# Kernel tuning notes

Hardware: AMD Instinct MI355X
Metric: run time of the kernel (lower is better)

Reference implementation:

```python
import jax, jax.numpy as jnp
import numpy as np

NUM_HEADS = 16
LN_EPS = 1e-05


def setup_inputs() -> dict:
    key = jax.random.key(0)
    ks = jax.random.split(key, 10)
    B, S, H = 2, 2048, 1024
    s = 1.0 / np.sqrt(H)
    return {
        "hidden_states": jax.random.normal(ks[0], (B, S, H), dtype=jnp.float32),
        "Wq": jax.random.normal(ks[1], (H, H), dtype=jnp.float32) * s,
        "bq": jax.random.normal(ks[2], (H,), dtype=jnp.float32) * 0.02,
        "Wk": jax.random.normal(ks[3], (H, H), dtype=jnp.float32) * s,
        "bk": jax.random.normal(ks[4], (H,), dtype=jnp.float32) * 0.02,
        "Wv": jax.random.normal(ks[5], (H, H), dtype=jnp.float32) * s,
        "bv": jax.random.normal(ks[6], (H,), dtype=jnp.float32) * 0.02,
        "Wd": jax.random.normal(ks[7], (H, H), dtype=jnp.float32) * s,
        "bd": jax.random.normal(ks[8], (H,), dtype=jnp.float32) * 0.02,
        "ln_gamma": jnp.ones((H,), dtype=jnp.float32),
        "ln_beta": jnp.zeros((H,), dtype=jnp.float32),
    }


def reference(hidden_states, Wq, bq, Wk, bk, Wv, bv, Wd, bd, ln_gamma, ln_beta):
    B, S, H = hidden_states.shape
    nh = NUM_HEADS
    hd = H // nh

    # QKV projections (torch Linear: x @ W.T + b), split heads -> [B, nh, S, hd]
    def proj(W, b):
        y = jnp.einsum('bsh,oh->bso', hidden_states, W) + b
        return y.reshape(B, S, nh, hd).transpose(0, 2, 1, 3)

    q = proj(Wq, bq)
    k = proj(Wk, bk)
    v = proj(Wv, bv)

    # scaled dot-product attention: [B, nh, S, S]
    scores = jnp.einsum('bhqd,bhkd->bhqk', q, k) / jnp.sqrt(jnp.float32(hd))
    probs = jax.nn.softmax(scores, axis=-1)
    ctx = jnp.einsum('bhqk,bhkd->bhqd', probs, v)  # [B, nh, S, hd]
    ctx = ctx.transpose(0, 2, 1, 3).reshape(B, S, H)

    # output dense + residual + LayerNorm
    attn_out = jnp.einsum('bsh,oh->bso', ctx, Wd) + bd
    x = attn_out + hidden_states
    mu = jnp.mean(x, axis=-1, keepdims=True)
    var = jnp.mean(jnp.square(x - mu), axis=-1, keepdims=True)
    return (x - mu) * jax.lax.rsqrt(var + LN_EPS) * ln_gamma + ln_beta
```

## Files before the change

kernel.cpp:

```cpp
#include <hip/hip_runtime.h>

constexpr int kH    = 1024;
constexpr int kSEQ  = 2048;
constexpr int kBATCH= 2;
constexpr int kNH   = 16;
constexpr int kHD   = 64;
constexpr int kM    = 4096;

typedef _Float16 h8  __attribute__((ext_vector_type(8)));
typedef _Float16 h4  __attribute__((ext_vector_type(4)));
typedef float   f32x4 __attribute__((ext_vector_type(4)));

static __device__ __forceinline__ f32x4 mfma16(h8 a, h8 b, f32x4 c) {
  return __builtin_amdgcn_mfma_f32_16x16x32_f16(a, b, c, 0, 0, 0);
}

static __device__ __forceinline__ void gll16(const _Float16* g, _Float16* l) {
  __builtin_amdgcn_global_load_lds(
      (const __attribute__((address_space(1))) void*)g,
      (__attribute__((address_space(3))) void*)l, 16, 0, 0);
}

#define QSCALE 0.18033688011112042f
#define C0INIT (-5.770780163555854f)

__global__ __launch_bounds__(256) void cvt_all(
    const float* __restrict__ X,  const float* __restrict__ Wq,
    const float* __restrict__ Wk, const float* __restrict__ Wv,
    const float* __restrict__ Wd,
    _Float16* __restrict__ Xh,  _Float16* __restrict__ Wqh,
    _Float16* __restrict__ Wkh, _Float16* __restrict__ Wvh,
    _Float16* __restrict__ Wdh)
{
  int i = blockIdx.x * 256 + threadIdx.x;
  const float* src; _Float16* dst; int off;
  if (i < (kM * kH) / 4) {
    src = X; dst = Xh; off = i;
  } else {
    int j = i - (kM * kH) / 4;
    int w = j >> 18;
    off = j & 262143;
    src = (w == 0) ? Wq : (w == 1) ? Wk : (w == 2) ? Wv : Wd;
    dst = (w == 0) ? Wqh : (w == 1) ? Wkh : (w == 2) ? Wvh : Wdh;
  }
  float4 v = reinterpret_cast<const float4*>(src)[off];
  h4 o;
  o[0] = (_Float16)v.x; o[1] = (_Float16)v.y;
  o[2] = (_Float16)v.z; o[3] = (_Float16)v.w;
  reinterpret_cast<h4*>(dst)[off] = o;
}

__global__ __launch_bounds__(256, 2) void qkv_gemm(
    const _Float16* __restrict__ Xh,
    const _Float16* __restrict__ Wq, const _Float16* __restrict__ Wk,
    const _Float16* __restrict__ Wv,
    const float* __restrict__ bq, const float* __restrict__ bk,
    const float* __restrict__ bv,
    _Float16* __restrict__ Qo, _Float16* __restrict__ Ko, _Float16* __restrict__ Vo)
{
  const int proj = blockIdx.z;
  const _Float16* W   = (proj == 0) ? Wq : ((proj == 1) ? Wk : Wv);
  const float*    bias= (proj == 0) ? bq : ((proj == 1) ? bk : bv);
  _Float16*       Out = (proj == 0) ? Qo : ((proj == 1) ? Ko : Vo);

  const int m0 = blockIdx.y * 128, n0 = blockIdx.x * 128;
  __shared__ __align__(16) _Float16 As[2][128 * 32];
  __shared__ __align__(16) _Float16 Bs[2][128 * 32];

  const int tid  = threadIdx.x;
  const int wave = tid >> 6, lane = tid & 63, quad = lane >> 4, l16 = lane & 15;
  const int mw = (wave & 1) * 64, nw = (wave >> 1) * 64;

  f32x4 acc[4][4] = {};
  const int grow = wave * 32 + (lane >> 2);
  const int gcol = (lane & 3) * 8;
  const _Float16* Ag = Xh + (size_t)(m0 + grow) * kH + gcol;
  const _Float16* Bg = W  + (size_t)(n0 + grow) * kH + gcol;

  {
    gll16(Ag,            &As[0][wave * 1024]);
    gll16(Ag + 16 * kH,  &As[0][wave * 1024 + 512]);
    gll16(Bg,            &Bs[0][wave * 1024]);
    gll16(Bg + 16 * kH,  &Bs[0][wave * 1024 + 512]);
  }

  for (int k = 0; k < 32; ++k) {
    const int cur = k & 1;
    __syncthreads();
    if (k < 31) {
      const int k0 = (k + 1) * 32, nb = cur ^ 1;
      gll16(Ag + k0,           &As[nb][wave * 1024]);
      gll16(Ag + 16 * kH + k0, &As[nb][wave * 1024 + 512]);
      gll16(Bg + k0,           &Bs[nb][wave * 1024]);
      gll16(Bg + 16 * kH + k0, &Bs[nb][wave * 1024 + 512]);
    }
    h8 af[4], bf[4];
    #pragma unroll
    for (int mi = 0; mi < 4; ++mi)
      af[mi] = *reinterpret_cast<const h8*>(&As[cur][(mw + mi * 16 + l16) * 32 + quad * 8]);
    #pragma unroll
    for (int ni = 0; ni < 4; ++ni)
      bf[ni] = *reinterpret_cast<const h8*>(&Bs[cur][(nw + ni * 16 + l16) * 32 + quad * 8]);
    #pragma unroll
    for (int mi = 0; mi < 4; ++mi)
      #pragma unroll
      for (int ni = 0; ni < 4; ++ni)
        acc[mi][ni] = mfma16(af[mi], bf[ni], acc[mi][ni]);
  }

  #pragma unroll
  for (int mi = 0; mi < 4; ++mi)
  #pragma unroll
  for (int ni = 0; ni < 4; ++ni) {
    const int ng = n0 + nw + ni * 16 + l16;
    const float bv_ = bias[ng];
    const int hh = ng >> 6, dd = ng & 63;
    #pragma unroll
    for (int r = 0; r < 4; ++r) {
      const int mg = m0 + mw + mi * 16 + quad * 4 + r;
      float val = acc[mi][ni][r] + bv_;
      if (proj == 0) val *= QSCALE;
      const int bb = mg >> 11, srow = mg & 2047;
      Out[(((size_t)(bb * kNH + hh) * kSEQ) + srow) * kHD + dd] = (_Float16)val;
    }
  }
}

__global__ __launch_bounds__(256) void vtrans(const _Float16* __restrict__ V,
                                              _Float16* __restrict__ Vt)
{
  const int st = blockIdx.x;
  const int bh = blockIdx.y;
  __shared__ __align__(16) _Float16 Lt[64][72];
  const int t = threadIdx.x, r = t >> 2, c = (t & 3) * 16;
  const _Float16* src = V + (size_t)bh * kSEQ * kHD + (size_t)(st * 64 + r) * kHD + c;
  h8 p0 = *reinterpret_cast<const h8*>(src);
  h8 p1 = *reinterpret_cast<const h8*>(src + 8);
  #pragma unroll
  for (int e = 0; e < 8; ++e) Lt[c + e][r] = p0[e];
  #pragma unroll
  for (int e = 0; e < 8; ++e) Lt[c + 8 + e][r] = p1[e];
  __syncthreads();
  _Float16* dst = Vt + (size_t)bh * kHD * kSEQ + (size_t)r * kSEQ + st * 64 + c;
  *reinterpret_cast<h8*>(dst)     = *reinterpret_cast<const h8*>(&Lt[r][c]);
  *reinterpret_cast<h8*>(dst + 8) = *reinterpret_cast<const h8*>(&Lt[r][c + 8]);
}

__global__ __launch_bounds__(512, 4) void attn_kernel(
    const _Float16* __restrict__ Q, const _Float16* __restrict__ K,
    const _Float16* __restrict__ Vt, _Float16* __restrict__ Ctx)
{
  const int qt = blockIdx.x, bh = blockIdx.y;
  const int tid = threadIdx.x;
  const int wave = tid >> 6, lane = tid & 63, quad = lane >> 4, l16 = lane & 15;
  const int sw = l16 & 7;

  __shared__ __align__(16) _Float16 Kl[2][64 * 64];
  __shared__ __align__(16) _Float16 Vl[2][64 * 64];
  __shared__ __align__(16) _Float16 Pl[8][16 * 64];

  const _Float16* Qb = Q  + (size_t)bh * kSEQ * kHD;
  const _Float16* Kb = K  + (size_t)bh * kSEQ * kHD;
  const _Float16* Vb = Vt + (size_t)bh * kHD * kSEQ;

  const int qbase = qt * 128 + wave * 16;
  h8 qf[2];
  #pragma unroll
  for (int dh = 0; dh < 2; ++dh)
    qf[dh] = *reinterpret_cast<const h8*>(
        &Qb[(size_t)(qbase + l16) * kHD + dh * 32 + quad * 8]);

  const int srow0  = lane >> 3;
  const int schunk = (lane & 7) ^ srow0;
  const int krow   = wave * 8 + srow0;
  const _Float16* Kg = Kb + (size_t)krow * kHD + schunk * 8;
  const _Float16* Vg = Vb + (size_t)krow * kSEQ + schunk * 8;
  _Float16* PlW = Pl[wave];

  float l_acc = 0.f;
  f32x4 o[4] = {};

  {
    gll16(Kg, &Kl[0][(wave * 8) * 64]);
    gll16(Vg, &Vl[0][(wave * 8) * 64]);
  }

  for (int kt = 0; kt < kSEQ / 64; ++kt) {
    const int cur = kt & 1;
    __syncthreads();
    if (kt + 1 < kSEQ / 64) {
      const int nb = cur ^ 1;
      const size_t ko = (size_t)(kt + 1) * 64;
      gll16(Kg + ko * kHD, &Kl[nb][(wave * 8) * 64]);
      gll16(Vg + ko,       &Vl[nb][(wave * 8) * 64]);
    }
    const _Float16* Kc = Kl[cur];
    const _Float16* Vc = Vl[cur];

    h8 ka[4][2];
    #pragma unroll
    for (int nt = 0; nt < 4; ++nt) {
      const int keyl = nt * 16 + l16;
      ka[nt][0] = *reinterpret_cast<const h8*>(&Kc[keyl * 64 + ((quad     ) ^ sw) * 8]);
      ka[nt][1] = *reinterpret_cast<const h8*>(&Kc[keyl * 64 + ((quad ^ 4) ^ sw) * 8]);
    }
    f32x4 s[4];
    __builtin_amdgcn_s_setprio(1);
    #pragma unroll
    for (int nt = 0; nt < 4; ++nt) {
      f32x4 a = {C0INIT, C0INIT, C0INIT, C0INIT};
      a = mfma16(ka[nt][0], qf[0], a);
      a = mfma16(ka[nt][1], qf[1], a);
      s[nt] = a;
    }
    __builtin_amdgcn_s_setprio(0);

    #pragma unroll
    for (int nt = 0; nt < 4; ++nt) {
      float e0 = exp2f(s[nt][0]);
      float e1 = exp2f(s[nt][1]);
      float e2 = exp2f(s[nt][2]);
      float e3 = exp2f(s[nt][3]);
      l_acc += (e0 + e1) + (e2 + e3);
      h4 pp;
      pp[0] = (_Float16)e0; pp[1] = (_Float16)e1;
      pp[2] = (_Float16)e2; pp[3] = (_Float16)e3;
      const int c8 = (nt * 2 + (quad >> 1)) ^ sw;
      *reinterpret_cast<h4*>(&PlW[l16 * 64 + c8 * 8 + (quad & 1) * 4]) = pp;
    }

    #pragma unroll
    for (int kc = 0; kc < 2; ++kc) {
      const int cs = ((kc * 4 + quad) ^ sw) * 8;
      h8 pa = *reinterpret_cast<const h8*>(&PlW[l16 * 64 + cs]);
      h8 vb0 = *reinterpret_cast<const h8*>(&Vc[(0 * 16 + l16) * 64 + cs]);
      h8 vb1 = *reinterpret_cast<const h8*>(&Vc[(1 * 16 + l16) * 64 + cs]);
      h8 vb2 = *reinterpret_cast<const h8*>(&Vc[(2 * 16 + l16) * 64 + cs]);
      h8 vb3 = *reinterpret_cast<const h8*>(&Vc[(3 * 16 + l16) * 64 + cs]);
      __builtin_amdgcn_s_setprio(1);
      o[0] = mfma16(pa, vb0, o[0]);
      o[1] = mfma16(pa, vb1, o[1]);
      o[2] = mfma16(pa, vb2, o[2]);
      o[3] = mfma16(pa, vb3, o[3]);
      __builtin_amdgcn_s_setprio(0);
    }
  }

  float li = l_acc;
  li += __shfl_xor(li, 16);
  li += __shfl_xor(li, 32);
  li = 1.f / li;
  const int b = bh >> 4, hh = bh & 15;
  #pragma unroll
  for (int r = 0; r < 4; ++r) {
    const float linv = __shfl(li, quad * 4 + r);
    const int srow = qbase + quad * 4 + r;
    #pragma unroll
    for (int dt = 0; dt < 4; ++dt) {
      const int col = hh * kHD + dt * 16 + l16;
      Ctx[((size_t)(b * kSEQ + srow)) * kH + col] = (_Float16)(o[dt][r] * linv);
    }
  }
}

__global__ __launch_bounds__(256, 2) void dense_gemm(
    const _Float16* __restrict__ A, const _Float16* __restrict__ W,
    const float* __restrict__ bias, const float* __restrict__ resid,
    float* __restrict__ Out)
{
  const int m0 = blockIdx.y * 128, n0 = blockIdx.x * 64;
  __shared__ __align__(16) _Float16 As[2][128 * 32];
  __shared__ __align__(16) _Float16 Bs[2][64 * 32];
  const int tid  = threadIdx.x;
  const int wave = tid >> 6, lane = tid & 63, quad = lane >> 4, l16 = lane & 15;
  const int mw = (wave & 1) * 64, nw = (wave >> 1) * 32;
  f32x4 acc[4][2] = {};
  const int growA = wave * 32 + (lane >> 2);
  const int growB = wave * 16 + (lane >> 2);
  const int gcol = (lane & 3) * 8;
  const _Float16* Ag = A + (size_t)(m0 + growA) * kH + gcol;
  const _Float16* Bg = W + (size_t)(n0 + growB) * kH + gcol;

  {
    gll16(Ag,           &As[0][wave * 1024]);
    gll16(Ag + 16 * kH, &As[0][wave * 1024 + 512]);
    gll16(Bg,           &Bs[0][wave * 512]);
  }

  for (int k = 0; k < 32; ++k) {
    const int cur = k & 1;
    __syncthreads();
    if (k < 31) {
      const int k0 = (k + 1) * 32, nb = cur ^ 1;
      gll16(Ag + k0,           &As[nb][wave * 1024]);
      gll16(Ag + 16 * kH + k0, &As[nb][wave * 1024 + 512]);
      gll16(Bg + k0,           &Bs[nb][wave * 512]);
    }
    h8 af[4], bf[2];
    #pragma unroll
    for (int mi = 0; mi < 4; ++mi)
      af[mi] = *reinterpret_cast<const h8*>(&As[cur][(mw + mi * 16 + l16) * 32 + quad * 8]);
    #pragma unroll
    for (int ni = 0; ni < 2; ++ni)
      bf[ni] = *reinterpret_cast<const h8*>(&Bs[cur][(nw + ni * 16 + l16) * 32 + quad * 8]);
    #pragma unroll
    for (int mi = 0; mi < 4; ++mi)
      #pragma unroll
      for (int ni = 0; ni < 2; ++ni)
        acc[mi][ni] = mfma16(af[mi], bf[ni], acc[mi][ni]);
  }
  #pragma unroll
  for (int mi = 0; mi < 4; ++mi)
  #pragma unroll
  for (int ni = 0; ni < 2; ++ni) {
    const int ng = n0 + nw + ni * 16 + l16;
    const float bv_ = bias[ng];
    #pragma unroll
    for (int r = 0; r < 4; ++r) {
      const int mg = m0 + mw + mi * 16 + quad * 4 + r;
      Out[(size_t)mg * kH + ng] = acc[mi][ni][r] + bv_ + resid[(size_t)mg * kH + ng];
    }
  }
}

__global__ __launch_bounds__(256) void ln_kernel(const float* __restrict__ Tmp,
    const float* __restrict__ gamma, const float* __restrict__ beta,
    float* __restrict__ out)
{
  const int row = blockIdx.x;
  const float4 v = reinterpret_cast<const float4*>(Tmp + (size_t)row * kH)[threadIdx.x];
  float s  = v.x + v.y + v.z + v.w;
  float ss = v.x * v.x + v.y * v.y + v.z * v.z + v.w * v.w;
  #pragma unroll
  for (int off = 32; off > 0; off >>= 1) {
    s  += __shfl_down(s, off);
    ss += __shfl_down(ss, off);
  }
  __shared__ float red[8];
  const int wave = threadIdx.x >> 6, lane = threadIdx.x & 63;
  if (lane == 0) { red[wave] = s; red[4 + wave] = ss; }
  __syncthreads();
  s  = red[0] + red[1] + red[2] + red[3];
  ss = red[4] + red[5] + red[6] + red[7];
  const float mu   = s * (1.f / kH);
  const float var  = ss * (1.f / kH) - mu * mu;
  const float rstd = rsqrtf(var + 1e-5f);
  const float4 g  = reinterpret_cast<const float4*>(gamma)[threadIdx.x];
  const float4 bb = reinterpret_cast<const float4*>(beta)[threadIdx.x];
  float4 o;
  o.x = (v.x - mu) * rstd * g.x + bb.x;
  o.y = (v.y - mu) * rstd * g.y + bb.y;
  o.z = (v.z - mu) * rstd * g.z + bb.z;
  o.w = (v.w - mu) * rstd * g.w + bb.w;
  reinterpret_cast<float4*>(out + (size_t)row * kH)[threadIdx.x] = o;
}

extern "C" void kernel_launch(void* const* d_in, const int* in_sizes, int n_in,
                              void* d_out, int out_size, void* d_ws, size_t ws_size,
                              hipStream_t stream) {
  const float* hs    = (const float*)d_in[0];
  const float* Wq    = (const float*)d_in[1];
  const float* bq    = (const float*)d_in[2];
  const float* Wk    = (const float*)d_in[3];
  const float* bk    = (const float*)d_in[4];
  const float* Wv    = (const float*)d_in[5];
  const float* bv    = (const float*)d_in[6];
  const float* Wd    = (const float*)d_in[7];
  const float* bd    = (const float*)d_in[8];
  const float* gamma = (const float*)d_in[9];
  const float* beta  = (const float*)d_in[10];
  float* out = (float*)d_out;

  char* ws = (char*)d_ws;
  _Float16* Xh  = (_Float16*)(ws + 0);
  _Float16* Wqh = (_Float16*)(ws + 8388608);
  _Float16* Wkh = (_Float16*)(ws + 10485760);
  _Float16* Wvh = (_Float16*)(ws + 12582912);
  _Float16* Wdh = (_Float16*)(ws + 14680064);
  _Float16* Qh  = (_Float16*)(ws + 16777216);
  _Float16* Kh  = (_Float16*)(ws + 25165824);
  _Float16* Vh  = (_Float16*)(ws + 33554432);
  _Float16* Ch  = (_Float16*)(ws + 41943040);
  _Float16* Vtb = Xh;
  float*    Tmp = (float*)Qh;

  cvt_all<<<8192, 256, 0, stream>>>(hs, Wq, Wk, Wv, Wd, Xh, Wqh, Wkh, Wvh, Wdh);
  qkv_gemm<<<dim3(kH / 128, kM / 128, 3), 256, 0, stream>>>(
      Xh, Wqh, Wkh, Wvh, bq, bk, bv, Qh, Kh, Vh);
  vtrans<<<dim3(kSEQ / 64, kBATCH * kNH), 256, 0, stream>>>(Vh, Vtb);
  attn_kernel<<<dim3(kSEQ / 128, kBATCH * kNH), 512, 0, stream>>>(Qh, Kh, Vtb, Ch);
  dense_gemm<<<dim3(kH / 64, kM / 128), 256, 0, stream>>>(Ch, Wdh, bd, hs, Tmp);
  ln_kernel<<<kM, 256, 0, stream>>>(Tmp, gamma, beta, out);
}
```

Before: 220.2 us.

## Split attention key tile across wave groups with 32-row queries and LDS reduction

```diff
diff --git a/kernel.cpp b/kernel.cpp
--- a/kernel.cpp
+++ b/kernel.cpp
@@ -154,36 +154,41 @@
   const int tid = threadIdx.x;
   const int wave = tid >> 6, lane = tid & 63, quad = lane >> 4, l16 = lane & 15;
   const int sw = l16 & 7;
-
-  __shared__ __align__(16) _Float16 Kl[2][64 * 64];
-  __shared__ __align__(16) _Float16 Vl[2][64 * 64];
-  __shared__ __align__(16) _Float16 Pl[8][16 * 64];
+  const int qw = wave & 3;
+  const int wg = wave >> 2;
+
+  __shared__ __align__(16) char smem[53248];
+  _Float16* const Kl = (_Float16*)smem;
+  _Float16* const Vl = (_Float16*)(smem + 16384);
+  _Float16* const Pl = (_Float16*)(smem + 32768);
+  float* const Ored = (float*)smem;
+  float* const Lred = (float*)(smem + 34816);
 
   const _Float16* Qb = Q  + (size_t)bh * kSEQ * kHD;
   const _Float16* Kb = K  + (size_t)bh * kSEQ * kHD;
   const _Float16* Vb = Vt + (size_t)bh * kHD * kSEQ;
 
-  const int qbase = qt * 128 + wave * 16;
-  h8 qf[2];
-  #pragma unroll
-  for (int dh = 0; dh < 2; ++dh)
-    qf[dh] = *reinterpret_cast<const h8*>(
-        &Qb[(size_t)(qbase + l16) * kHD + dh * 32 + quad * 8]);
+  const int qbase = qt * 128 + qw * 32;
+  h8 qf[2][2];
+  #pragma unroll
+  for (int qh = 0; qh < 2; ++qh)
+    #pragma unroll
+    for (int dh = 0; dh < 2; ++dh)
+      qf[qh][dh] = *reinterpret_cast<const h8*>(
+          &Qb[(size_t)(qbase + qh * 16 + l16) * kHD + dh * 32 + quad * 8]);
 
   const int srow0  = lane >> 3;
   const int schunk = (lane & 7) ^ srow0;
   const int krow   = wave * 8 + srow0;
   const _Float16* Kg = Kb + (size_t)krow * kHD + schunk * 8;
   const _Float16* Vg = Vb + (size_t)krow * kSEQ + schunk * 8;
-  _Float16* PlW = Pl[wave];
-
-  float l_acc = 0.f;
-  f32x4 o[4] = {};
-
-  {
-    gll16(Kg, &Kl[0][(wave * 8) * 64]);
-    gll16(Vg, &Vl[0][(wave * 8) * 64]);
-  }
+  _Float16* const PlW = Pl + wave * 1280;
+
+  float l_acc[2] = {0.f, 0.f};
+  f32x4 o[2][4] = {};
+
+  gll16(Kg, &Kl[(wave * 8) * 64]);
+  gll16(Vg, &Vl[(wave * 8) * 64]);
 
   for (int kt = 0; kt < kSEQ / 64; ++kt) {
     const int cur = kt & 1;
@@ -191,76 +196,119 @@
     if (kt + 1 < kSEQ / 64) {
       const int nb = cur ^ 1;
       const size_t ko = (size_t)(kt + 1) * 64;
-      gll16(Kg + ko * kHD, &Kl[nb][(wave * 8) * 64]);
-      gll16(Vg + ko,       &Vl[nb][(wave * 8) * 64]);
-    }
-    const _Float16* Kc = Kl[cur];
-    const _Float16* Vc = Vl[cur];
-
-    h8 ka[4][2];
-    #pragma unroll
-    for (int nt = 0; nt < 4; ++nt) {
-      const int keyl = nt * 16 + l16;
-      ka[nt][0] = *reinterpret_cast<const h8*>(&Kc[keyl * 64 + ((quad     ) ^ sw) * 8]);
+      gll16(Kg + ko * kHD, &Kl[nb * 4096 + (wave * 8) * 64]);
+      gll16(Vg + ko,       &Vl[nb * 4096 + (wave * 8) * 64]);
+    }
+    const _Float16* Kc = Kl + cur * 4096;
+    const _Float16* Vc = Vl + cur * 4096;
+
+    h8 ka[2][2];
+    #pragma unroll
+    for (int nt = 0; nt < 2; ++nt) {
+      const int keyl = wg * 32 + nt * 16 + l16;
+      ka[nt][0] = *reinterpret_cast<const h8*>(&Kc[keyl * 64 + ((quad    ) ^ sw) * 8]);
       ka[nt][1] = *reinterpret_cast<const h8*>(&Kc[keyl * 64 + ((quad ^ 4) ^ sw) * 8]);
     }
-    f32x4 s[4];
+    f32x4 s[2][2];
     __builtin_amdgcn_s_setprio(1);
     #pragma unroll
-    for (int nt = 0; nt < 4; ++nt) {
-      f32x4 a = {C0INIT, C0INIT, C0INIT, C0INIT};
-      a = mfma16(ka[nt][0], qf[0], a);
-      a = mfma16(ka[nt][1], qf[1], a);
-      s[nt] = a;
-    }
+    for (int nt = 0; nt < 2; ++nt)
+      #pragma unroll
+      for (int qh = 0; qh < 2; ++qh) {
+        f32x4 a = {C0INIT, C0INIT, C0INIT, C0INIT};
+        a = mfma16(ka[nt][0], qf[qh][0], a);
+        a = mfma16(ka[nt][1], qf[qh][1], a);
+        s[nt][qh] = a;
+      }
     __builtin_amdgcn_s_setprio(0);
 
     #pragma unroll
-    for (int nt = 0; nt < 4; ++nt) {
-      float e0 = exp2f(s[nt][0]);
-      float e1 = exp2f(s[nt][1]);
-      float e2 = exp2f(s[nt][2]);
-      float e3 = exp2f(s[nt][3]);
-      l_acc += (e0 + e1) + (e2 + e3);
-      h4 pp;
-      pp[0] = (_Float16)e0; pp[1] = (_Float16)e1;
-      pp[2] = (_Float16)e2; pp[3] = (_Float16)e3;
-      const int c8 = (nt * 2 + (quad >> 1)) ^ sw;
-      *reinterpret_cast<h4*>(&PlW[l16 * 64 + c8 * 8 + (quad & 1) * 4]) = pp;
-    }
-
-    #pragma unroll
-    for (int kc = 0; kc < 2; ++kc) {
-      const int cs = ((kc * 4 + quad) ^ sw) * 8;
-      h8 pa = *reinterpret_cast<const h8*>(&PlW[l16 * 64 + cs]);
-      h8 vb0 = *reinterpret_cast<const h8*>(&Vc[(0 * 16 + l16) * 64 + cs]);
-      h8 vb1 = *reinterpret_cast<const h8*>(&Vc[(1 * 16 + l16) * 64 + cs]);
-      h8 vb2 = *reinterpret_cast<const h8*>(&Vc[(2 * 16 + l16) * 64 + cs]);
-      h8 vb3 = *reinterpret_cast<const h8*>(&Vc[(3 * 16 + l16) * 64 + cs]);
-      __builtin_amdgcn_s_setprio(1);
-      o[0] = mfma16(pa, vb0, o[0]);
-      o[1] = mfma16(pa, vb1, o[1]);
-      o[2] = mfma16(pa, vb2, o[2]);
-      o[3] = mfma16(pa, vb3, o[3]);
-      __builtin_amdgcn_s_setprio(0);
-    }
-  }
-
-  float li = l_acc;
-  li += __shfl_xor(li, 16);
-  li += __shfl_xor(li, 32);
-  li = 1.f / li;
+    for (int nt = 0; nt < 2; ++nt)
+      #pragma unroll
+      for (int qh = 0; qh < 2; ++qh) {
+        float e0 = exp2f(s[nt][qh][0]);
+        float e1 = exp2f(s[nt][qh][1]);
+        float e2 = exp2f(s[nt][qh][2]);
+        float e3 = exp2f(s[nt][qh][3]);
+        l_acc[qh] += (e0 + e1) + (e2 + e3);
+        h4 pp;
+        pp[0] = (_Float16)e0; pp[1] = (_Float16)e1;
+        pp[2] = (_Float16)e2; pp[3] = (_Float16)e3;
+        const int c = nt * 2 + (quad >> 1);
+        *reinterpret_cast<h4*>(&PlW[(qh * 16 + l16) * 40 + c * 8 + (quad & 1) * 4]) = pp;
+      }
+
+    h8 pa0 = *reinterpret_cast<const h8*>(&PlW[(     l16) * 40 + quad * 8]);
+    h8 pa1 = *reinterpret_cast<const h8*>(&PlW[(16 + l16) * 40 + quad * 8]);
+    const int cs = ((wg * 4 + quad) ^ sw) * 8;
+    h8 vb0 = *reinterpret_cast<const h8*>(&Vc[(0 * 16 + l16) * 64 + cs]);
+    h8 vb1 = *reinterpret_cast<const h8*>(&Vc[(1 * 16 + l16) * 64 + cs]);
+    h8 vb2 = *reinterpret_cast<const h8*>(&Vc[(2 * 16 + l16) * 64 + cs]);
+    h8 vb3 = *reinterpret_cast<const h8*>(&Vc[(3 * 16 + l16) * 64 + cs]);
+    __builtin_amdgcn_s_setprio(1);
+    o[0][0] = mfma16(pa0, vb0, o[0][0]);
+    o[1][0] = mfma16(pa1, vb0, o[1][0]);
+    o[0][1] = mfma16(pa0, vb1, o[0][1]);
+    o[1][1] = mfma16(pa1, vb1, o[1][1]);
+    o[0][2] = mfma16(pa0, vb2, o[0][2]);
+    o[1][2] = mfma16(pa1, vb2, o[1][2]);
+    o[0][3] = mfma16(pa0, vb3, o[0][3]);
+    o[1][3] = mfma16(pa1, vb3, o[1][3]);
+    __builtin_amdgcn_s_setprio(0);
+  }
+
+  float li[2] = {l_acc[0], l_acc[1]};
+  #pragma unroll
+  for (int qh = 0; qh < 2; ++qh) {
+    li[qh] += __shfl_xor(li[qh], 16);
+    li[qh] += __shfl_xor(li[qh], 32);
+  }
+
+  __syncthreads();
+  if (wg == 1) {
+    float* myO = Ored + (qw * 64 + lane) * 34;
+    #pragma unroll
+    for (int qh = 0; qh < 2; ++qh)
+      #pragma unroll
+      for (int dt = 0; dt < 4; ++dt) {
+        reinterpret_cast<float2*>(&myO[qh * 16 + dt * 4])[0] =
+            reinterpret_cast<const float2*>(&o[qh][dt])[0];
+        reinterpret_cast<float2*>(&myO[qh * 16 + dt * 4 + 2])[0] =
+            reinterpret_cast<const float2*>(&o[qh][dt])[1];
+      }
+    if (quad == 0) {
+      Lred[(qw * 2 + 0) * 16 + l16] = li[0];
+      Lred[(qw * 2 + 1) * 16 + l16] = li[1];
+    }
+  }
+  __syncthreads();
+  if (wg == 1) return;
+
+  const float* pO = Ored + (qw * 64 + lane) * 34;
+  #pragma unroll
+  for (int qh = 0; qh < 2; ++qh) {
+    #pragma unroll
+    for (int dt = 0; dt < 4; ++dt) {
+      float2 a = reinterpret_cast<const float2*>(&pO[qh * 16 + dt * 4])[0];
+      float2 b2 = reinterpret_cast<const float2*>(&pO[qh * 16 + dt * 4 + 2])[0];
+      o[qh][dt][0] += a.x;  o[qh][dt][1] += a.y;
+      o[qh][dt][2] += b2.x; o[qh][dt][3] += b2.y;
+    }
+    li[qh] = 1.f / (li[qh] + Lred[(qw * 2 + qh) * 16 + l16]);
+  }
   const int b = bh >> 4, hh = bh & 15;
   #pragma unroll
-  for (int r = 0; r < 4; ++r) {
-    const float linv = __shfl(li, quad * 4 + r);
-    const int srow = qbase + quad * 4 + r;
-    #pragma unroll
-    for (int dt = 0; dt < 4; ++dt) {
-      const int col = hh * kHD + dt * 16 + l16;
-      Ctx[((size_t)(b * kSEQ + srow)) * kH + col] = (_Float16)(o[dt][r] * linv);
-    }
-  }
+  for (int qh = 0; qh < 2; ++qh)
+    #pragma unroll
+    for (int r = 0; r < 4; ++r) {
+      const float linv = __shfl(li[qh], quad * 4 + r);
+      const int srow = qbase + qh * 16 + quad * 4 + r;
+      #pragma unroll
+      for (int dt = 0; dt < 4; ++dt) {
+        const int col = hh * kHD + dt * 16 + l16;
+        Ctx[((size_t)(b * kSEQ + srow)) * kH + col] = (_Float16)(o[qh][dt][r] * linv);
+      }
+    }
 }
 
 __global__ __launch_bounds__(256, 2) void dense_gemm(
```

Result: no change. 218.5 us (-0.8%).
